# Performance work log

Measured on AMD Instinct MI355X. Metric: run time of the kernel, lower is better.

## Reference

```python
import jax, jax.numpy as jnp
import numpy as np

N_NODES = 100000


def gcn_conv(x, src, dst, dinv, W, b):
    # PyG GCNConv: h = D^-1/2 (A+I) D^-1/2 (x W) + b
    h = x @ W                                   # [N, out]
    norm = dinv[src] * dinv[dst]                # [E'] edge weights
    msg = norm[:, None] * h[src]                # gather + scale
    agg = jax.ops.segment_sum(msg, dst, num_segments=x.shape[0])
    return agg + b


def setup_inputs() -> dict:
    key = jax.random.key(0)
    ks = jax.random.split(key, 8)
    x = jax.random.normal(ks[0], (N_NODES, 64), dtype=jnp.float32)
    edge_index = jax.random.randint(ks[1], (2, 1600000), 0, N_NODES, dtype=jnp.int32)
    s = 0.1
    return {
        "x": x,
        "edge_index": edge_index,
        "W1": jax.random.normal(ks[2], (64, 64), dtype=jnp.float32) * s,
        "b1": jnp.zeros((64,), dtype=jnp.float32),
        "W2": jax.random.normal(ks[3], (64, 32), dtype=jnp.float32) * s,
        "b2": jnp.zeros((32,), dtype=jnp.float32),
        "W3": jax.random.normal(ks[4], (32, 2), dtype=jnp.float32) * s,
        "b3": jnp.zeros((2,), dtype=jnp.float32),
    }


def reference(x, edge_index, W1, b1, W2, b2, W3, b3):
    n = x.shape[0]
    loop = jnp.arange(n, dtype=edge_index.dtype)
    src = jnp.concatenate([edge_index[0], loop])  # add self-loops
    dst = jnp.concatenate([edge_index[1], loop])
    deg = jax.ops.segment_sum(jnp.ones_like(dst, dtype=x.dtype), dst, num_segments=n)
    dinv = jnp.where(deg > 0, jax.lax.rsqrt(jnp.maximum(deg, 1.0)), 0.0)
    h = jax.nn.relu(gcn_conv(x, src, dst, dinv, W1, b1))
    h = jax.nn.relu(gcn_conv(h, src, dst, dinv, W2, b2))
    return gcn_conv(h, src, dst, dinv, W3, b3)
```

## Files before the change

### kernel.cpp

```cpp
#include <hip/hip_runtime.h>
#include <hip/hip_fp16.h>

#define N_NODES 100000
#define N_EDGES 1600000
#define BSHIFT 9
#define NBUCK ((N_NODES + 511) / 512)
#define BCAP 12288

__global__ void bucket1_kernel(const int* __restrict__ src, const int* __restrict__ dst,
                               int* __restrict__ gbcount, int2* __restrict__ bbuf, int E) {
    __shared__ int hcnt[NBUCK];
    __shared__ int hbase[NBUCK];
    int t = threadIdx.x;
    for (int i = t; i < NBUCK; i += 256) hcnt[i] = 0;
    __syncthreads();
    int e0 = blockIdx.x * 2048 + t;
    int ss[8], dd[8];
#pragma unroll
    for (int u = 0; u < 8; u++) {
        int e = e0 + u * 256;
        if (e < E) {
            ss[u] = src[e];
            dd[u] = dst[e];
            atomicAdd(&hcnt[dd[u] >> BSHIFT], 1);
        } else {
            dd[u] = -1;
        }
    }
    __syncthreads();
    for (int i = t; i < NBUCK; i += 256) {
        int c = hcnt[i];
        hbase[i] = c ? atomicAdd(&gbcount[i], c) : 0;
        hcnt[i] = 0;
    }
    __syncthreads();
#pragma unroll
    for (int u = 0; u < 8; u++) {
        if (dd[u] >= 0) {
            int bk = dd[u] >> BSHIFT;
            int r = atomicAdd(&hcnt[bk], 1);
            bbuf[(size_t)bk * BCAP + hbase[bk] + r] = make_int2(ss[u], dd[u]);
        }
    }
}

__global__ void scan196_kernel(const int* __restrict__ gbcount, int* __restrict__ gbase,
                               int* __restrict__ rowptrN, int E) {
    __shared__ int s[256];
    int t = threadIdx.x;
    int v = (t < NBUCK) ? gbcount[t] : 0;
    s[t] = v;
    __syncthreads();
    for (int off = 1; off < 256; off <<= 1) {
        int u = (t >= off) ? s[t - off] : 0;
        __syncthreads();
        s[t] += u;
        __syncthreads();
    }
    if (t < NBUCK) gbase[t] = s[t] - v;
    if (t == 0) *rowptrN = E;
}

__global__ __launch_bounds__(512)
void bucket2_kernel(const int2* __restrict__ bbuf, const int* __restrict__ gbcount,
                    const int* __restrict__ gbase, int* __restrict__ rowptr,
                    float* __restrict__ dinv, int* __restrict__ eidx, int N) {
    int b = blockIdx.x;
    int base_node = b << BSHIFT;
    int nn = min(512, N - base_node);
    int t = threadIdx.x;
    __shared__ int s[512];
    __shared__ int cur[512];
    s[t] = 0;
    __syncthreads();
    int sz = gbcount[b];
    const int2* eb = bbuf + (size_t)b * BCAP;
    for (int j = t; j < sz; j += 512) atomicAdd(&s[eb[j].y - base_node], 1);
    __syncthreads();
    int myc = s[t];
    if (t < nn) dinv[base_node + t] = rsqrtf((float)myc + 1.0f);
    __syncthreads();
    for (int off = 1; off < 512; off <<= 1) {
        int u = (t >= off) ? s[t - off] : 0;
        __syncthreads();
        s[t] += u;
        __syncthreads();
    }
    int rp = gbase[b] + s[t] - myc;
    if (t < nn) rowptr[base_node + t] = rp;
    cur[t] = rp;
    __syncthreads();
    for (int j = t; j < sz; j += 512) {
        int2 e = eb[j];
        int pos = atomicAdd(&cur[e.y - base_node], 1);
        eidx[pos] = e.x;
    }
}

__global__ void sortrow_wave(const int* __restrict__ rowptr, int* __restrict__ eidx, int n) {
    int g = (blockIdx.x * blockDim.x + threadIdx.x) >> 6;
    int lane = threadIdx.x & 63;
    if (g >= n) return;
    int start = rowptr[g];
    int end = rowptr[g + 1];
    int len = end - start;
    if (len <= 1) return;

    if (len <= 64) {
        int v = (lane < len) ? eidx[start + lane] : 0x7fffffff;
#pragma unroll
        for (int k = 2; k <= 64; k <<= 1) {
#pragma unroll
            for (int j = k >> 1; j > 0; j >>= 1) {
                int partner = __shfl_xor(v, j, 64);
                bool up = ((lane & k) == 0);
                bool keepMin = (((lane & j) == 0) == up);
                int mn = min(v, partner), mx = max(v, partner);
                v = keepMin ? mn : mx;
            }
        }
        if (lane < len) eidx[start + lane] = v;
    } else if (lane == 0) {
        for (int i = start + 1; i < end; i++) {
            int key = eidx[i];
            int j = i - 1;
            while (j >= start && eidx[j] > key) { eidx[j + 1] = eidx[j]; j--; }
            eidx[j + 1] = key;
        }
    }
}

template <int FIN, int FOUT, typename TO>
__global__ __launch_bounds__(256, 2)
void gemm_tiled(const float* __restrict__ in, const float* __restrict__ W,
                const float* __restrict__ dinv, TO* __restrict__ out, int n) {
    constexpr int CG = FOUT / 4;
    constexpr int RG = 256 / CG;
    constexpr int TR = RG * 4;
    constexpr int LDA = FIN + 4;
    __shared__ float sIn[TR * LDA];
    __shared__ float sW[FIN * FOUT];

    for (int i = threadIdx.x; i < FIN * FOUT / 4; i += 256)
        ((float4*)sW)[i] = ((const float4*)W)[i];

    int r0 = blockIdx.x * TR;
    for (int i = threadIdx.x; i < TR * FIN / 4; i += 256) {
        int rr = i / (FIN / 4);
        int cc = i % (FIN / 4);
        int gr = r0 + rr;
        float4 v = (gr < n) ? ((const float4*)in)[(size_t)gr * (FIN / 4) + cc]
                            : make_float4(0.f, 0.f, 0.f, 0.f);
        *(float4*)&sIn[rr * LDA + cc * 4] = v;
    }
    __syncthreads();

    int tc = threadIdx.x % CG;
    int tr = threadIdx.x / CG;
    int rbase = tr * 4, cbase = tc * 4;
    float acc[4][4] = {};

#pragma unroll 2
    for (int k = 0; k < FIN; k += 4) {
        float4 a[4], b[4];
#pragma unroll
        for (int i = 0; i < 4; i++) a[i] = *(float4*)&sIn[(rbase + i) * LDA + k];
#pragma unroll
        for (int kk = 0; kk < 4; kk++) b[kk] = *(float4*)&sW[(k + kk) * FOUT + cbase];
#pragma unroll
        for (int i = 0; i < 4; i++) {
            acc[i][0] += a[i].x * b[0].x + a[i].y * b[1].x + a[i].z * b[2].x + a[i].w * b[3].x;
            acc[i][1] += a[i].x * b[0].y + a[i].y * b[1].y + a[i].z * b[2].y + a[i].w * b[3].y;
            acc[i][2] += a[i].x * b[0].z + a[i].y * b[1].z + a[i].z * b[2].z + a[i].w * b[3].z;
            acc[i][3] += a[i].x * b[0].w + a[i].y * b[1].w + a[i].z * b[2].w + a[i].w * b[3].w;
        }
    }

#pragma unroll
    for (int i = 0; i < 4; i++) {
        int gr = r0 + rbase + i;
        if (gr < n) {
            float dv = dinv[gr];
            if constexpr (sizeof(TO) == 2) {
                union { __half h[4]; uint2 u; } pk;
                pk.h[0] = __float2half_rn(dv * acc[i][0]);
                pk.h[1] = __float2half_rn(dv * acc[i][1]);
                pk.h[2] = __float2half_rn(dv * acc[i][2]);
                pk.h[3] = __float2half_rn(dv * acc[i][3]);
                *(uint2*)&out[(size_t)gr * FOUT + cbase] = pk.u;
            } else {
                *(float4*)&out[(size_t)gr * FOUT + cbase] =
                    make_float4(dv * acc[i][0], dv * acc[i][1], dv * acc[i][2], dv * acc[i][3]);
            }
        }
    }
}

template <int FIN, int FOUT>
__global__ void gemm_kernel(const float* __restrict__ in, const float* __restrict__ W,
                            const float* __restrict__ dinv, float* __restrict__ out, int n) {
    __shared__ float sW[FIN * FOUT];
    for (int i = threadIdx.x; i < FIN * FOUT; i += blockDim.x) sW[i] = W[i];
    __syncthreads();
    constexpr int ROWS = 256 / FOUT;
    int r = blockIdx.x * ROWS + threadIdx.x / FOUT;
    int c = threadIdx.x % FOUT;
    if (r >= n) return;
    float acc = 0.f;
#pragma unroll
    for (int k = 0; k < FIN; k++) acc += in[r * FIN + k] * sW[k * FOUT + c];
    out[r * FOUT + c] = dinv[r] * acc;
}

template <int F, bool RELU>
__global__ __launch_bounds__(256, 4)
void agg_vec_kernel(const int* __restrict__ eidx, const int* __restrict__ rowptr,
                    const float* __restrict__ dinv, const __half* __restrict__ h,
                    const float* __restrict__ bias, float* __restrict__ out, int n) {
    constexpr int L = 8;
    constexpr int PH = F / L;
    using vh = _Float16 __attribute__((ext_vector_type(PH)));
    int g = (blockIdx.x * blockDim.x + threadIdx.x) / L;
    int lane = threadIdx.x % L;
    if (g >= n) return;
    int j = rowptr[g];
    int end = rowptr[g + 1];
    float di = dinv[g];
    const __half* hb = h + lane * PH;

    float acc0[PH], acc1[PH];
#pragma unroll
    for (int q = 0; q < PH; q++) { acc0[q] = 0.f; acc1[q] = 0.f; }

    for (; j + 8 <= end; j += 8) {
        int s0 = eidx[j];
        int s1 = eidx[j + 1];
        int s2 = eidx[j + 2];
        int s3 = eidx[j + 3];
        int s4 = eidx[j + 4];
        int s5 = eidx[j + 5];
        int s6 = eidx[j + 6];
        int s7 = eidx[j + 7];
        vh v0 = *(const vh*)(hb + (size_t)s0 * F);
        vh v1 = *(const vh*)(hb + (size_t)s1 * F);
        vh v2 = *(const vh*)(hb + (size_t)s2 * F);
        vh v3 = *(const vh*)(hb + (size_t)s3 * F);
        vh v4 = *(const vh*)(hb + (size_t)s4 * F);
        vh v5 = *(const vh*)(hb + (size_t)s5 * F);
        vh v6 = *(const vh*)(hb + (size_t)s6 * F);
        vh v7 = *(const vh*)(hb + (size_t)s7 * F);
#pragma unroll
        for (int q = 0; q < PH; q++) {
            acc0[q] += (float)v0[q] + (float)v2[q];
            acc1[q] += (float)v1[q] + (float)v3[q];
            acc0[q] += (float)v4[q] + (float)v6[q];
            acc1[q] += (float)v5[q] + (float)v7[q];
        }
    }
    for (; j + 2 <= end; j += 2) {
        int s0 = eidx[j];
        int s1 = eidx[j + 1];
        vh v0 = *(const vh*)(hb + (size_t)s0 * F);
        vh v1 = *(const vh*)(hb + (size_t)s1 * F);
#pragma unroll
        for (int q = 0; q < PH; q++) { acc0[q] += (float)v0[q]; acc1[q] += (float)v1[q]; }
    }
    if (j < end) {
        vh v = *(const vh*)(hb + (size_t)eidx[j] * F);
#pragma unroll
        for (int q = 0; q < PH; q++) acc0[q] += (float)v[q];
    }

    vh sv = *(const vh*)(hb + (size_t)g * F);
    float res[PH];
#pragma unroll
    for (int q = 0; q < PH; q++) {
        float v = di * ((acc0[q] + acc1[q]) + (float)sv[q]) + bias[lane * PH + q];
        res[q] = RELU ? fmaxf(v, 0.f) : v;
    }
    float* ob = out + (size_t)g * F + lane * PH;
#pragma unroll
    for (int q = 0; q < PH; q += 4)
        *(float4*)(ob + q) = make_float4(res[q], res[q + 1], res[q + 2], res[q + 3]);
}

template <int F, bool RELU>
__global__ void agg_kernel(const int* __restrict__ eidx, const int* __restrict__ rowptr,
                           const float* __restrict__ dinv, const float* __restrict__ h,
                           const float* __restrict__ b, float* __restrict__ out, int n) {
    int g = (blockIdx.x * blockDim.x + threadIdx.x) / F;
    int lane = threadIdx.x % F;
    if (g >= n) return;
    int j = rowptr[g];
    int end = rowptr[g + 1];
    float di = dinv[g];
    float hs = h[(size_t)g * F + lane];

    float acc0 = 0.f, acc1 = 0.f, acc2 = 0.f, acc3 = 0.f;
    float acc4 = 0.f, acc5 = 0.f, acc6 = 0.f, acc7 = 0.f;
    for (; j + 8 <= end; j += 8) {
        int s0 = eidx[j];
        int s1 = eidx[j + 1];
        int s2 = eidx[j + 2];
        int s3 = eidx[j + 3];
        int s4 = eidx[j + 4];
        int s5 = eidx[j + 5];
        int s6 = eidx[j + 6];
        int s7 = eidx[j + 7];
        acc0 += h[(size_t)s0 * F + lane];
        acc1 += h[(size_t)s1 * F + lane];
        acc2 += h[(size_t)s2 * F + lane];
        acc3 += h[(size_t)s3 * F + lane];
        acc4 += h[(size_t)s4 * F + lane];
        acc5 += h[(size_t)s5 * F + lane];
        acc6 += h[(size_t)s6 * F + lane];
        acc7 += h[(size_t)s7 * F + lane];
    }
    for (; j + 2 <= end; j += 2) {
        int s0 = eidx[j];
        int s1 = eidx[j + 1];
        acc0 += h[(size_t)s0 * F + lane];
        acc1 += h[(size_t)s1 * F + lane];
    }
    if (j < end) {
        acc2 += h[(size_t)eidx[j] * F + lane];
    }
    float acc = ((acc0 + acc1) + (acc2 + acc3)) + ((acc4 + acc5) + (acc6 + acc7));
    float v = di * (acc + hs) + b[lane];
    out[(size_t)g * F + lane] = RELU ? fmaxf(v, 0.f) : v;
}

extern "C" void kernel_launch(void* const* d_in, const int* in_sizes, int n_in,
                              void* d_out, int out_size, void* d_ws, size_t ws_size,
                              hipStream_t stream) {
    const float* x  = (const float*)d_in[0];
    const int* ei   = (const int*)d_in[1];
    const float* W1 = (const float*)d_in[2];
    const float* b1 = (const float*)d_in[3];
    const float* W2 = (const float*)d_in[4];
    const float* b2 = (const float*)d_in[5];
    const float* W3 = (const float*)d_in[6];
    const float* b3 = (const float*)d_in[7];
    float* out = (float*)d_out;

    const int N = N_NODES;
    const int E = N_EDGES;
    const int* src = ei;
    const int* dst = ei + E;

    char* p = (char*)d_ws;
    int*   rowptr  = (int*)p;             p += ((size_t)(N + 1) * 4 + 15) / 16 * 16;
    float* dinv    = (float*)p;           p += ((size_t)N * 4 + 15) / 16 * 16;
    int*   gbcount = (int*)p;             p += ((size_t)NBUCK * 4 + 15) / 16 * 16;
    int*   gbase   = (int*)p;             p += ((size_t)NBUCK * 4 + 15) / 16 * 16;
    int*   eidx    = (int*)p;             p += (size_t)E * 4;
    __half* A      = (__half*)p;          p += (size_t)N * 64 * 2;
    float* B       = (float*)p;
    int2*  bbuf    = (int2*)B;
    float* A3      = (float*)A;

    const int T = 256;

    hipMemsetAsync(gbcount, 0, NBUCK * sizeof(int), stream);
    bucket1_kernel<<<(E + 2047) / 2048, T, 0, stream>>>(src, dst, gbcount, bbuf, E);
    scan196_kernel<<<1, 256, 0, stream>>>(gbcount, gbase, rowptr + N, E);
    bucket2_kernel<<<NBUCK, 512, 0, stream>>>(bbuf, gbcount, gbase, rowptr, dinv, eidx, N);
    sortrow_wave<<<(N * 64 + T - 1) / T, T, 0, stream>>>(rowptr, eidx, N);

    gemm_tiled<64, 64, __half><<<(N + 63) / 64, T, 0, stream>>>(x, W1, dinv, A, N);
    agg_vec_kernel<64, true><<<(N * 8 + T - 1) / T, T, 0, stream>>>(eidx, rowptr, dinv, A, b1, B, N);

    gemm_tiled<64, 32, __half><<<(N + 127) / 128, T, 0, stream>>>(B, W2, dinv, A, N);
    agg_vec_kernel<32, true><<<(N * 8 + T - 1) / T, T, 0, stream>>>(eidx, rowptr, dinv, A, b2, B, N);

    gemm_kernel<32, 2><<<(N + 127) / 128, T, 0, stream>>>(B, W3, dinv, A3, N);
    agg_kernel<2, false><<<(N * 2 + T - 1) / T, T, 0, stream>>>(eidx, rowptr, dinv, A3, b3, out, N);
}
```

Baseline: 287.1 us.

## Fuse aggregation with next-layer GEMM and pack bucket edges into one int

Merges each layer's neighbour aggregation with the following layer's small dense transform. The aggregated, ReLU'd row is staged in shared memory and multiplied by W2 or W3 in the same kernel, so the fp32 intermediate activations no longer round-trip through global memory and two launches disappear. The bucketing pass now packs source id and local destination offset into one 32-bit word, halving scratch traffic. The packing relies on node ids fitting in 17 bits, and the fused GEMM runs at low per-thread arithmetic density, which could cost some compute efficiency.

```diff
diff --git a/kernel.cpp b/kernel.cpp
--- a/kernel.cpp
+++ b/kernel.cpp
@@ -8,7 +8,7 @@
 #define BCAP 12288
 
 __global__ void bucket1_kernel(const int* __restrict__ src, const int* __restrict__ dst,
-                               int* __restrict__ gbcount, int2* __restrict__ bbuf, int E) {
+                               int* __restrict__ gbcount, int* __restrict__ bbuf, int E) {
     __shared__ int hcnt[NBUCK];
     __shared__ int hbase[NBUCK];
     int t = threadIdx.x;
@@ -39,7 +39,7 @@
         if (dd[u] >= 0) {
             int bk = dd[u] >> BSHIFT;
             int r = atomicAdd(&hcnt[bk], 1);
-            bbuf[(size_t)bk * BCAP + hbase[bk] + r] = make_int2(ss[u], dd[u]);
+            bbuf[(size_t)bk * BCAP + hbase[bk] + r] = ss[u] | ((dd[u] & 511) << 17);
         }
     }
 }
@@ -62,7 +62,7 @@
 }
 
 __global__ __launch_bounds__(512)
-void bucket2_kernel(const int2* __restrict__ bbuf, const int* __restrict__ gbcount,
+void bucket2_kernel(const int* __restrict__ bbuf, const int* __restrict__ gbcount,
                     const int* __restrict__ gbase, int* __restrict__ rowptr,
                     float* __restrict__ dinv, int* __restrict__ eidx, int N) {
     int b = blockIdx.x;
@@ -74,8 +74,8 @@
     s[t] = 0;
     __syncthreads();
     int sz = gbcount[b];
-    const int2* eb = bbuf + (size_t)b * BCAP;
-    for (int j = t; j < sz; j += 512) atomicAdd(&s[eb[j].y - base_node], 1);
+    const int* eb = bbuf + (size_t)b * BCAP;
+    for (int j = t; j < sz; j += 512) atomicAdd(&s[((unsigned)eb[j]) >> 17], 1);
     __syncthreads();
     int myc = s[t];
     if (t < nn) dinv[base_node + t] = rsqrtf((float)myc + 1.0f);
@@ -91,9 +91,9 @@
     cur[t] = rp;
     __syncthreads();
     for (int j = t; j < sz; j += 512) {
-        int2 e = eb[j];
-        int pos = atomicAdd(&cur[e.y - base_node], 1);
-        eidx[pos] = e.x;
+        int e = eb[j];
+        int pos = atomicAdd(&cur[((unsigned)e) >> 17], 1);
+        eidx[pos] = e & 0x1FFFF;
     }
 }
 
@@ -130,10 +130,10 @@
     }
 }
 
-template <int FIN, int FOUT, typename TO>
+template <int FIN, int FOUT>
 __global__ __launch_bounds__(256, 2)
 void gemm_tiled(const float* __restrict__ in, const float* __restrict__ W,
-                const float* __restrict__ dinv, TO* __restrict__ out, int n) {
+                const float* __restrict__ dinv, __half* __restrict__ out, int n) {
     constexpr int CG = FOUT / 4;
     constexpr int RG = 256 / CG;
     constexpr int TR = RG * 4;
@@ -181,110 +181,121 @@
         int gr = r0 + rbase + i;
         if (gr < n) {
             float dv = dinv[gr];
-            if constexpr (sizeof(TO) == 2) {
-                union { __half h[4]; uint2 u; } pk;
-                pk.h[0] = __float2half_rn(dv * acc[i][0]);
-                pk.h[1] = __float2half_rn(dv * acc[i][1]);
-                pk.h[2] = __float2half_rn(dv * acc[i][2]);
-                pk.h[3] = __float2half_rn(dv * acc[i][3]);
-                *(uint2*)&out[(size_t)gr * FOUT + cbase] = pk.u;
-            } else {
-                *(float4*)&out[(size_t)gr * FOUT + cbase] =
-                    make_float4(dv * acc[i][0], dv * acc[i][1], dv * acc[i][2], dv * acc[i][3]);
-            }
-        }
-    }
-}
-
-template <int FIN, int FOUT>
-__global__ void gemm_kernel(const float* __restrict__ in, const float* __restrict__ W,
-                            const float* __restrict__ dinv, float* __restrict__ out, int n) {
+            union { __half h[4]; uint2 u; } pk;
+            pk.h[0] = __float2half_rn(dv * acc[i][0]);
+            pk.h[1] = __float2half_rn(dv * acc[i][1]);
+            pk.h[2] = __float2half_rn(dv * acc[i][2]);
+            pk.h[3] = __float2half_rn(dv * acc[i][3]);
+            *(uint2*)&out[(size_t)gr * FOUT + cbase] = pk.u;
+        }
+    }
+}
+
+template <int FIN, int FOUT, bool OUT_HALF>
+__global__ __launch_bounds__(256, 4)
+void agg_gemm_kernel(const int* __restrict__ eidx, const int* __restrict__ rowptr,
+                     const float* __restrict__ dinv, const __half* __restrict__ h,
+                     const float* __restrict__ bias, const float* __restrict__ W,
+                     void* __restrict__ outv, int n) {
+    constexpr int L = 8;
+    constexpr int PH = FIN / L;
+    constexpr int NODES = 256 / L;
+    using vh = _Float16 __attribute__((ext_vector_type(PH)));
     __shared__ float sW[FIN * FOUT];
-    for (int i = threadIdx.x; i < FIN * FOUT; i += blockDim.x) sW[i] = W[i];
-    __syncthreads();
-    constexpr int ROWS = 256 / FOUT;
-    int r = blockIdx.x * ROWS + threadIdx.x / FOUT;
-    int c = threadIdx.x % FOUT;
-    if (r >= n) return;
-    float acc = 0.f;
-#pragma unroll
-    for (int k = 0; k < FIN; k++) acc += in[r * FIN + k] * sW[k * FOUT + c];
-    out[r * FOUT + c] = dinv[r] * acc;
-}
-
-template <int F, bool RELU>
-__global__ __launch_bounds__(256, 4)
-void agg_vec_kernel(const int* __restrict__ eidx, const int* __restrict__ rowptr,
-                    const float* __restrict__ dinv, const __half* __restrict__ h,
-                    const float* __restrict__ bias, float* __restrict__ out, int n) {
-    constexpr int L = 8;
-    constexpr int PH = F / L;
-    using vh = _Float16 __attribute__((ext_vector_type(PH)));
+    __shared__ float sv[NODES * FIN];
+
+    for (int i = threadIdx.x; i < FIN * FOUT / 4; i += 256)
+        ((float4*)sW)[i] = ((const float4*)W)[i];
+
     int g = (blockIdx.x * blockDim.x + threadIdx.x) / L;
     int lane = threadIdx.x % L;
-    if (g >= n) return;
-    int j = rowptr[g];
-    int end = rowptr[g + 1];
-    float di = dinv[g];
-    const __half* hb = h + lane * PH;
-
-    float acc0[PH], acc1[PH];
-#pragma unroll
-    for (int q = 0; q < PH; q++) { acc0[q] = 0.f; acc1[q] = 0.f; }
-
-    for (; j + 8 <= end; j += 8) {
-        int s0 = eidx[j];
-        int s1 = eidx[j + 1];
-        int s2 = eidx[j + 2];
-        int s3 = eidx[j + 3];
-        int s4 = eidx[j + 4];
-        int s5 = eidx[j + 5];
-        int s6 = eidx[j + 6];
-        int s7 = eidx[j + 7];
-        vh v0 = *(const vh*)(hb + (size_t)s0 * F);
-        vh v1 = *(const vh*)(hb + (size_t)s1 * F);
-        vh v2 = *(const vh*)(hb + (size_t)s2 * F);
-        vh v3 = *(const vh*)(hb + (size_t)s3 * F);
-        vh v4 = *(const vh*)(hb + (size_t)s4 * F);
-        vh v5 = *(const vh*)(hb + (size_t)s5 * F);
-        vh v6 = *(const vh*)(hb + (size_t)s6 * F);
-        vh v7 = *(const vh*)(hb + (size_t)s7 * F);
+    int slot = threadIdx.x / L;
+    float di = 0.f;
+
+    if (g < n) {
+        int j = rowptr[g];
+        int end = rowptr[g + 1];
+        di = dinv[g];
+        const __half* hb = h + lane * PH;
+
+        float acc0[PH], acc1[PH];
+#pragma unroll
+        for (int q = 0; q < PH; q++) { acc0[q] = 0.f; acc1[q] = 0.f; }
+
+        for (; j + 8 <= end; j += 8) {
+            int s0 = eidx[j];
+            int s1 = eidx[j + 1];
+            int s2 = eidx[j + 2];
+            int s3 = eidx[j + 3];
+            int s4 = eidx[j + 4];
+            int s5 = eidx[j + 5];
+            int s6 = eidx[j + 6];
+            int s7 = eidx[j + 7];
+            vh v0 = *(const vh*)(hb + (size_t)s0 * FIN);
+            vh v1 = *(const vh*)(hb + (size_t)s1 * FIN);
+            vh v2 = *(const vh*)(hb + (size_t)s2 * FIN);
+            vh v3 = *(const vh*)(hb + (size_t)s3 * FIN);
+            vh v4 = *(const vh*)(hb + (size_t)s4 * FIN);
+            vh v5 = *(const vh*)(hb + (size_t)s5 * FIN);
+            vh v6 = *(const vh*)(hb + (size_t)s6 * FIN);
+            vh v7 = *(const vh*)(hb + (size_t)s7 * FIN);
+#pragma unroll
+            for (int q = 0; q < PH; q++) {
+                acc0[q] += (float)v0[q] + (float)v2[q];
+                acc1[q] += (float)v1[q] + (float)v3[q];
+                acc0[q] += (float)v4[q] + (float)v6[q];
+                acc1[q] += (float)v5[q] + (float)v7[q];
+            }
+        }
+        for (; j + 2 <= end; j += 2) {
+            int s0 = eidx[j];
+            int s1 = eidx[j + 1];
+            vh v0 = *(const vh*)(hb + (size_t)s0 * FIN);
+            vh v1 = *(const vh*)(hb + (size_t)s1 * FIN);
+#pragma unroll
+            for (int q = 0; q < PH; q++) { acc0[q] += (float)v0[q]; acc1[q] += (float)v1[q]; }
+        }
+        if (j < end) {
+            vh v = *(const vh*)(hb + (size_t)eidx[j] * FIN);
+#pragma unroll
+            for (int q = 0; q < PH; q++) acc0[q] += (float)v[q];
+        }
+
+        vh sf = *(const vh*)(hb + (size_t)g * FIN);
+        float* svn = &sv[slot * FIN + lane * PH];
 #pragma unroll
         for (int q = 0; q < PH; q++) {
-            acc0[q] += (float)v0[q] + (float)v2[q];
-            acc1[q] += (float)v1[q] + (float)v3[q];
-            acc0[q] += (float)v4[q] + (float)v6[q];
-            acc1[q] += (float)v5[q] + (float)v7[q];
-        }
-    }
-    for (; j + 2 <= end; j += 2) {
-        int s0 = eidx[j];
-        int s1 = eidx[j + 1];
-        vh v0 = *(const vh*)(hb + (size_t)s0 * F);
-        vh v1 = *(const vh*)(hb + (size_t)s1 * F);
-#pragma unroll
-        for (int q = 0; q < PH; q++) { acc0[q] += (float)v0[q]; acc1[q] += (float)v1[q]; }
-    }
-    if (j < end) {
-        vh v = *(const vh*)(hb + (size_t)eidx[j] * F);
-#pragma unroll
-        for (int q = 0; q < PH; q++) acc0[q] += (float)v[q];
-    }
-
-    vh sv = *(const vh*)(hb + (size_t)g * F);
-    float res[PH];
-#pragma unroll
-    for (int q = 0; q < PH; q++) {
-        float v = di * ((acc0[q] + acc1[q]) + (float)sv[q]) + bias[lane * PH + q];
-        res[q] = RELU ? fmaxf(v, 0.f) : v;
-    }
-    float* ob = out + (size_t)g * F + lane * PH;
-#pragma unroll
-    for (int q = 0; q < PH; q += 4)
-        *(float4*)(ob + q) = make_float4(res[q], res[q + 1], res[q + 2], res[q + 3]);
-}
-
-template <int F, bool RELU>
+            float v = di * ((acc0[q] + acc1[q]) + (float)sf[q]) + bias[lane * PH + q];
+            svn[q] = fmaxf(v, 0.f);
+        }
+    }
+    __syncthreads();
+
+    if (g < n) {
+        const float* vn = &sv[slot * FIN];
+        if constexpr (OUT_HALF) {
+            constexpr int PC = FOUT / L;
+            float o[PC] = {};
+            for (int k = 0; k < FIN; k++) {
+                float vk = vn[k];
+                float4 w = *(const float4*)&sW[k * FOUT + lane * PC];
+                o[0] += vk * w.x; o[1] += vk * w.y; o[2] += vk * w.z; o[3] += vk * w.w;
+            }
+            union { __half h[4]; uint2 u; } pk;
+#pragma unroll
+            for (int q = 0; q < PC; q++) pk.h[q] = __float2half_rn(di * o[q]);
+            *(uint2*)((__half*)outv + (size_t)g * FOUT + lane * PC) = pk.u;
+        } else {
+            if (lane < FOUT) {
+                float o = 0.f;
+                for (int k = 0; k < FIN; k++) o += vn[k] * sW[k * FOUT + lane];
+                ((float*)outv)[(size_t)g * FOUT + lane] = di * o;
+            }
+        }
+    }
+}
+
+template <int F>
 __global__ void agg_kernel(const int* __restrict__ eidx, const int* __restrict__ rowptr,
                            const float* __restrict__ dinv, const float* __restrict__ h,
                            const float* __restrict__ b, float* __restrict__ out, int n) {
@@ -326,8 +337,7 @@
         acc2 += h[(size_t)eidx[j] * F + lane];
     }
     float acc = ((acc0 + acc1) + (acc2 + acc3)) + ((acc4 + acc5) + (acc6 + acc7));
-    float v = di * (acc + hs) + b[lane];
-    out[(size_t)g * F + lane] = RELU ? fmaxf(v, 0.f) : v;
+    out[(size_t)g * F + lane] = di * (acc + hs) + b[lane];
 }
 
 extern "C" void kernel_launch(void* const* d_in, const int* in_sizes, int n_in,
@@ -349,15 +359,15 @@
     const int* dst = ei + E;
 
     char* p = (char*)d_ws;
-    int*   rowptr  = (int*)p;             p += ((size_t)(N + 1) * 4 + 15) / 16 * 16;
-    float* dinv    = (float*)p;           p += ((size_t)N * 4 + 15) / 16 * 16;
-    int*   gbcount = (int*)p;             p += ((size_t)NBUCK * 4 + 15) / 16 * 16;
-    int*   gbase   = (int*)p;             p += ((size_t)NBUCK * 4 + 15) / 16 * 16;
-    int*   eidx    = (int*)p;             p += (size_t)E * 4;
-    __half* A      = (__half*)p;          p += (size_t)N * 64 * 2;
-    float* B       = (float*)p;
-    int2*  bbuf    = (int2*)B;
-    float* A3      = (float*)A;
+    int*    rowptr  = (int*)p;            p += ((size_t)(N + 1) * 4 + 15) / 16 * 16;
+    float*  dinv    = (float*)p;          p += ((size_t)N * 4 + 15) / 16 * 16;
+    int*    gbcount = (int*)p;            p += ((size_t)NBUCK * 4 + 15) / 16 * 16;
+    int*    gbase   = (int*)p;            p += ((size_t)NBUCK * 4 + 15) / 16 * 16;
+    int*    eidx    = (int*)p;            p += (size_t)E * 4;
+    __half* A1      = (__half*)p;         p += (size_t)N * 64 * 2;
+    __half* A2      = (__half*)p;         p += (size_t)N * 32 * 2;
+    float*  A3      = (float*)p;          p += (size_t)N * 2 * 4;
+    int*    bbuf    = (int*)p;
 
     const int T = 256;
 
@@ -367,12 +377,13 @@
     bucket2_kernel<<<NBUCK, 512, 0, stream>>>(bbuf, gbcount, gbase, rowptr, dinv, eidx, N);
     sortrow_wave<<<(N * 64 + T - 1) / T, T, 0, stream>>>(rowptr, eidx, N);
 
-    gemm_tiled<64, 64, __half><<<(N + 63) / 64, T, 0, stream>>>(x, W1, dinv, A, N);
-    agg_vec_kernel<64, true><<<(N * 8 + T - 1) / T, T, 0, stream>>>(eidx, rowptr, dinv, A, b1, B, N);
-
-    gemm_tiled<64, 32, __half><<<(N + 127) / 128, T, 0, stream>>>(B, W2, dinv, A, N);
-    agg_vec_kernel<32, true><<<(N * 8 + T - 1) / T, T, 0, stream>>>(eidx, rowptr, dinv, A, b2, B, N);
-
-    gemm_kernel<32, 2><<<(N + 127) / 128, T, 0, stream>>>(B, W3, dinv, A3, N);
-    agg_kernel<2, false><<<(N * 2 + T - 1) / T, T, 0, stream>>>(eidx, rowptr, dinv, A3, b3, out, N);
-}
+    gemm_tiled<64, 64><<<(N + 63) / 64, T, 0, stream>>>(x, W1, dinv, A1, N);
+
+    agg_gemm_kernel<64, 32, true><<<(N + 31) / 32, T, 0, stream>>>(
+        eidx, rowptr, dinv, A1, b1, W2, A2, N);
+
+    agg_gemm_kernel<32, 2, false><<<(N + 31) / 32, T, 0, stream>>>(
+        eidx, rowptr, dinv, A2, b2, W3, A3, N);
+
+    agg_kernel<2><<<(N * 2 + T - 1) / T, T, 0, stream>>>(eidx, rowptr, dinv, A3, b3, out, N);
+}
```

Result: faster. 270.8 us (-5.7%).
